# Kernel tuning notes

Measured on AMD Instinct MI355X. Metric: run time of the kernel, lower is better.

Reference implementation:

```python
import jax, jax.numpy as jnp
import numpy as np

NHEAD = 8  # from init_kwargs
EPS = 1e-5  # nn.LayerNorm default


def _ln(x, w, b):
    mu = jnp.mean(x, axis=-1, keepdims=True)
    var = jnp.mean(jnp.square(x - mu), axis=-1, keepdims=True)
    return (x - mu) * jax.lax.rsqrt(var + EPS) * w + b


def setup_inputs() -> dict:
    key = jax.random.key(0)
    L, D, FF, B, S = 4, 256, 512, 2, 4096
    ks = jax.random.split(key, 14)
    s = 0.02
    inp = {
        "seq": jax.random.normal(ks[0], (B, S, D), jnp.float32),
        "Wqkv": jax.random.normal(ks[1], (L, 3 * D, D), jnp.float32) * s,
        "bqkv": jnp.zeros((L, 3 * D), jnp.float32),
        "Wo": jax.random.normal(ks[2], (L, D, D), jnp.float32) * s,
        "bo": jnp.zeros((L, D), jnp.float32),
        "ln1_w": jnp.ones((L, D), jnp.float32),
        "ln1_b": jnp.zeros((L, D), jnp.float32),
        "ln2_w": jnp.ones((L, D), jnp.float32),
        "ln2_b": jnp.zeros((L, D), jnp.float32),
        "W1": jax.random.normal(ks[3], (L, FF, D), jnp.float32) * s,
        "b1": jnp.zeros((L, FF), jnp.float32),
        "W2": jax.random.normal(ks[4], (L, D, FF), jnp.float32) * s,
        "b2": jnp.zeros((L, D), jnp.float32),
        "n_ctx": 2048,
    }
    return inp


def _forward(seq, Wqkv, bqkv, Wo, bo, ln1_w, ln1_b, ln2_w, ln2_b, W1, b1, W2, b2, n_ctx):
    B, S, D = seq.shape
    H = NHEAD
    hd = D // H
    scale = 1.0 / np.sqrt(hd).astype(np.float32)
    x = seq
    L = Wqkv.shape[0]
    for l in range(L):
        # pre-norm self-attention block (norm_first=True)
        h = _ln(x, ln1_w[l], ln1_b[l])
        qkv = h @ Wqkv[l].T + bqkv[l]            # [B,S,3D]
        q, k, v = jnp.split(qkv, 3, axis=-1)
        q = q.reshape(B, S, H, hd)
        # Mask structure: every token (context AND query) may only attend to
        # context keys [:n_ctx] -> keys/values restricted up-front, no dense
        # [S,S] score matrix and no explicit mask needed.
        kc = k[:, :n_ctx].reshape(B, n_ctx, H, hd)
        vc = v[:, :n_ctx].reshape(B, n_ctx, H, hd)
        scores = jnp.einsum('bqhd,bkhd->bhqk', q, kc) * scale  # [B,H,S,n_ctx]
        att = jax.nn.softmax(scores, axis=-1)
        o = jnp.einsum('bhqk,bkhd->bqhd', att, vc).reshape(B, S, D)
        x = x + o @ Wo[l].T + bo[l]
        # pre-norm feed-forward block, exact (erf) GELU as in PyTorch 'gelu'
        h2 = _ln(x, ln2_w[l], ln2_b[l])
        x = x + jax.nn.gelu(h2 @ W1[l].T + b1[l], approximate=False) @ W2[l].T + b2[l]
    return x


def reference(seq, Wqkv, bqkv, Wo, bo, ln1_w, ln1_b, ln2_w, ln2_b, W1, b1, W2, b2, n_ctx):
    return _forward(seq, Wqkv, bqkv, Wo, bo, ln1_w, ln1_b, ln2_w, ln2_b, W1, b1, W2, b2, n_ctx)
```

## Files before the change

kernel.cpp:

```cpp
#include <hip/hip_runtime.h>
#include <hip/hip_bf16.h>

#define BB 2
#define SS 4096
#define DD 256
#define FFD 512
#define NLAYER 4
#define NHEAD 8
#define HD 32
#define QKVD 768
#define NROWS 8192
#define NCTX 2048

typedef unsigned short u16;
typedef unsigned int   u32;
typedef __attribute__((ext_vector_type(8))) short short8;
typedef __attribute__((ext_vector_type(4))) float f32x4;

#if __has_builtin(__builtin_amdgcn_exp2f)
#define EXP2(x) __builtin_amdgcn_exp2f(x)
#else
#define EXP2(x) exp2f(x)
#endif

__device__ __forceinline__ float bf2f(u32 u) { return __uint_as_float(u << 16); }
__device__ __forceinline__ u16 f2bu(float f) {
    union { __hip_bfloat16 h; u16 u; } cv; cv.h = __float2bfloat16(f); return cv.u;
}
__device__ __forceinline__ float gelu_f(float v) {
    return 0.5f * v * (1.0f + erff(v * 0.70710678118654752f));
}

__global__ __launch_bounds__(256) void init_kernel(
        const float* __restrict__ s0, const float* __restrict__ s1,
        const float* __restrict__ s2, const float* __restrict__ s3,
        u16* __restrict__ d0, u16* __restrict__ d1,
        u16* __restrict__ d2, u16* __restrict__ d3,
        const float* __restrict__ seq, float* __restrict__ x,
        const float* __restrict__ lw, const float* __restrict__ lb,
        u16* __restrict__ hln) {
    int blk = blockIdx.x;
    if (blk < 2048) {
        const float* s; u16* d; int base;
        if (blk < 768)       { s = s0; d = d0; base = blk; }
        else if (blk < 1024) { s = s1; d = d1; base = blk - 768; }
        else if (blk < 1536) { s = s2; d = d2; base = blk - 1024; }
        else                 { s = s3; d = d3; base = blk - 1536; }
        int i = (base * 256 + threadIdx.x) * 4;
        float4 v = *reinterpret_cast<const float4*>(s + i);
        uint2 o;
        o.x = (u32)f2bu(v.x) | ((u32)f2bu(v.y) << 16);
        o.y = (u32)f2bu(v.z) | ((u32)f2bu(v.w) << 16);
        *reinterpret_cast<uint2*>(d + i) = o;
    } else {
        int row = (blk - 2048) * 4 + (threadIdx.x >> 6);
        int lane = threadIdx.x & 63;
        int c = lane * 4;
        float4 v = *reinterpret_cast<const float4*>(seq + (size_t)row * DD + c);
        *reinterpret_cast<float4*>(x + (size_t)row * DD + c) = v;
        float s  = v.x + v.y + v.z + v.w;
        float sq = v.x*v.x + v.y*v.y + v.z*v.z + v.w*v.w;
        #pragma unroll
        for (int off = 32; off >= 1; off >>= 1) {
            s  += __shfl_xor(s, off);
            sq += __shfl_xor(sq, off);
        }
        float mu   = s * (1.0f / DD);
        float var  = sq * (1.0f / DD) - mu * mu;
        float rstd = rsqrtf(var + 1e-5f);
        float4 wv = *reinterpret_cast<const float4*>(lw + c);
        float4 bv = *reinterpret_cast<const float4*>(lb + c);
        float o0 = (v.x - mu) * rstd * wv.x + bv.x;
        float o1 = (v.y - mu) * rstd * wv.y + bv.y;
        float o2 = (v.z - mu) * rstd * wv.z + bv.z;
        float o3 = (v.w - mu) * rstd * wv.w + bv.w;
        uint2 o;
        o.x = (u32)f2bu(o0) | ((u32)f2bu(o1) << 16);
        o.y = (u32)f2bu(o2) | ((u32)f2bu(o3) << 16);
        *reinterpret_cast<uint2*>(hln + (size_t)row * DD + c) = o;
    }
}

__global__ void ln_kernel(const float* __restrict__ x, const float* __restrict__ w,
                          const float* __restrict__ b, u16* __restrict__ out) {
    int row = blockIdx.x * 4 + (threadIdx.x >> 6);
    int lane = threadIdx.x & 63;
    int c = lane * 4;
    float4 v = *reinterpret_cast<const float4*>(x + (size_t)row * DD + c);
    float s  = v.x + v.y + v.z + v.w;
    float sq = v.x*v.x + v.y*v.y + v.z*v.z + v.w*v.w;
    #pragma unroll
    for (int off = 32; off >= 1; off >>= 1) {
        s  += __shfl_xor(s, off);
        sq += __shfl_xor(sq, off);
    }
    float mu   = s * (1.0f / DD);
    float var  = sq * (1.0f / DD) - mu * mu;
    float rstd = rsqrtf(var + 1e-5f);
    float4 wv = *reinterpret_cast<const float4*>(w + c);
    float4 bv = *reinterpret_cast<const float4*>(b + c);
    float o0 = (v.x - mu) * rstd * wv.x + bv.x;
    float o1 = (v.y - mu) * rstd * wv.y + bv.y;
    float o2 = (v.z - mu) * rstd * wv.z + bv.z;
    float o3 = (v.w - mu) * rstd * wv.w + bv.w;
    uint2 o;
    o.x = (u32)f2bu(o0) | ((u32)f2bu(o1) << 16);
    o.y = (u32)f2bu(o2) | ((u32)f2bu(o3) << 16);
    *reinterpret_cast<uint2*>(out + (size_t)row * DD + c) = o;
}

template<int TM, int ACT, int RES, int WV>
__global__ __launch_bounds__(256) void mfma_gemm(
        const u16* __restrict__ A, const u16* __restrict__ W, const float* __restrict__ bias,
        float* __restrict__ outf, u16* __restrict__ outb, u16* __restrict__ vtg,
        int N, int K) {
    constexpr int MI = TM / 32;
    __shared__ __align__(16) u16 As[TM][136];
    __shared__ __align__(16) u16 Ws[64][136];
    int tid = threadIdx.x;
    int wave = tid >> 6, lane = tid & 63, la = lane & 15, quad = lane >> 4;
    int wm = (wave & 1) * (TM / 2), wn = (wave >> 1) * 32;
    int m0 = blockIdx.y * TM, n0 = blockIdx.x * 64;
    f32x4 acc[MI][2];
    #pragma unroll
    for (int mi = 0; mi < MI; mi++)
        #pragma unroll
        for (int ni = 0; ni < 2; ni++)
            acc[mi][ni] = (f32x4){0.f, 0.f, 0.f, 0.f};

    int ar = tid >> 4, ac = (tid & 15) * 8;
    for (int k0 = 0; k0 < K; k0 += 128) {
        #pragma unroll
        for (int p = 0; p < TM / 16; p++)
            *reinterpret_cast<uint4*>(&As[ar + p*16][ac]) =
                *reinterpret_cast<const uint4*>(&A[(size_t)(m0 + ar + p*16) * K + k0 + ac]);
        #pragma unroll
        for (int p = 0; p < 4; p++)
            *reinterpret_cast<uint4*>(&Ws[ar + p*16][ac]) =
                *reinterpret_cast<const uint4*>(&W[(size_t)(n0 + ar + p*16) * K + k0 + ac]);
        __syncthreads();
        #pragma unroll
        for (int kh = 0; kh < 4; kh++) {
            short8 af[MI], bf[2];
            #pragma unroll
            for (int mi = 0; mi < MI; mi++)
                af[mi] = *reinterpret_cast<const short8*>(&As[wm + mi*16 + la][kh*32 + quad*8]);
            #pragma unroll
            for (int ni = 0; ni < 2; ni++)
                bf[ni] = *reinterpret_cast<const short8*>(&Ws[wn + ni*16 + la][kh*32 + quad*8]);
            #pragma unroll
            for (int mi = 0; mi < MI; mi++)
                #pragma unroll
                for (int ni = 0; ni < 2; ni++)
                    acc[mi][ni] = __builtin_amdgcn_mfma_f32_16x16x32_bf16(af[mi], bf[ni], acc[mi][ni], 0, 0, 0);
        }
        __syncthreads();
    }

    #pragma unroll
    for (int mi = 0; mi < MI; mi++) {
        #pragma unroll
        for (int ni = 0; ni < 2; ni++) {
            int n = n0 + wn + ni*16 + la;
            float bv = bias[n];
            #pragma unroll
            for (int r = 0; r < 4; r++) {
                int m = m0 + wm + mi*16 + quad*4 + r;
                float v = acc[mi][ni][r] + bv;
                if (ACT) v = gelu_f(v);
                if (RES) outf[(size_t)m * N + n] += v;
                else     outb[(size_t)m * N + n] = f2bu(v);
            }
        }
    }

    if (WV) {
        if ((n0 >= 2*DD) && ((m0 & (SS-1)) < NCTX)) {
            int b = m0 >> 12;
            int kb = ((m0 + wm) & (SS-1)) + quad*8;
            #pragma unroll
            for (int mi = 0; mi < MI; mi++) {
                int chunk = kb + (mi >> 1)*32 + (mi & 1)*4;
                #pragma unroll
                for (int ni = 0; ni < 2; ni++) {
                    int n = n0 + wn + ni*16 + la;
                    int vc = n - 2*DD;
                    float bv = bias[n];
                    u16* dst = &vtg[((size_t)((b << 3) + (vc >> 5)) * 32 + (vc & 31)) * NCTX + chunk];
                    uint2 w;
                    w.x = (u32)f2bu(acc[mi][ni][0] + bv) | ((u32)f2bu(acc[mi][ni][1] + bv) << 16);
                    w.y = (u32)f2bu(acc[mi][ni][2] + bv) | ((u32)f2bu(acc[mi][ni][3] + bv) << 16);
                    *reinterpret_cast<uint2*>(dst) = w;
                }
            }
        }
    }
}

#define SCL2 0.2550437f
#define SH2  11.5415603f
__global__ __launch_bounds__(512, 4) void mfma_attn(const u16* __restrict__ qkv,
                                                    const u16* __restrict__ vtg,
                                                    u16* __restrict__ out) {
    __shared__ __align__(16) u16 smem[18944];
    u16 (*Ks)[128][40] = reinterpret_cast<u16(*)[128][40]>(smem);
    u16 (*Vt)[32][136] = reinterpret_cast<u16(*)[32][136]>(smem + 10240);

    int tid = threadIdx.x;
    int wv = tid >> 6, lane = tid & 63, la = lane & 15, quad = lane >> 4;
    int qw = wv & 3, ksp = wv >> 2;
    int bh = blockIdx.y, qidx = blockIdx.x;
    int b = bh >> 3, hh = bh & 7;
    size_t tokbase = (size_t)b * SS;
    int qb = qidx * 128 + qw * 32;

    short8 qf[2];
    #pragma unroll
    for (int qt = 0; qt < 2; qt++) {
        uint4 u = *reinterpret_cast<const uint4*>(
            &qkv[(tokbase + qb + qt*16 + la) * QKVD + hh*32 + quad*8]);
        union { short8 v; u16 e[8]; } qa;
        u32 w[4] = {u.x, u.y, u.z, u.w};
        #pragma unroll
        for (int i = 0; i < 4; i++) {
            qa.e[2*i]   = f2bu(bf2f(w[i] & 0xffffu) * SCL2);
            qa.e[2*i+1] = f2bu(bf2f(w[i] >> 16) * SCL2);
        }
        qf[qt] = qa.v;
    }

    f32x4 o[2][2];
    #pragma unroll
    for (int i = 0; i < 2; i++)
        #pragma unroll
        for (int j = 0; j < 2; j++) o[i][j] = (f32x4){0.f, 0.f, 0.f, 0.f};
    f32x4 l_acc[2];
    l_acc[0] = (f32x4){0.f, 0.f, 0.f, 0.f};
    l_acc[1] = (f32x4){0.f, 0.f, 0.f, 0.f};
    const f32x4 cinit = (f32x4){-SH2, -SH2, -SH2, -SH2};
    short8 onesf;
    { union { short8 v; u16 e[8]; } t;
      #pragma unroll
      for (int i = 0; i < 8; i++) t.e[i] = 0x3F80;
      onesf = t.v; }

    int sr = tid >> 2, sk = (tid & 3) * 8;
    int vr = tid >> 4, vc = (tid & 15) * 8;
    const u16* kgp0 = &qkv[(tokbase + sr) * QKVD + DD + hh*32 + sk];
    const u16* kgp1 = &qkv[(tokbase + 1024 + sr) * QKVD + DD + hh*32 + sk];
    const u16* vgp  = &vtg[((size_t)bh*32 + vr) * NCTX + vc];
    uint4 kreg0 = *reinterpret_cast<const uint4*>(kgp0);
    uint4 kreg1 = *reinterpret_cast<const uint4*>(kgp1);
    uint4 vreg0 = *reinterpret_cast<const uint4*>(vgp);
    uint4 vreg1 = *reinterpret_cast<const uint4*>(vgp + 1024);

    for (int step = 0; step < 8; step++) {
        *reinterpret_cast<uint4*>(&Ks[0][sr][sk]) = kreg0;
        *reinterpret_cast<uint4*>(&Ks[1][sr][sk]) = kreg1;
        *reinterpret_cast<uint4*>(&Vt[0][vr][vc]) = vreg0;
        *reinterpret_cast<uint4*>(&Vt[1][vr][vc]) = vreg1;
        __syncthreads();
        if (step < 7) {
            kreg0 = *reinterpret_cast<const uint4*>(kgp0 + (size_t)(step+1)*128*QKVD);
            kreg1 = *reinterpret_cast<const uint4*>(kgp1 + (size_t)(step+1)*128*QKVD);
            vreg0 = *reinterpret_cast<const uint4*>(vgp + (step+1)*128);
            vreg1 = *reinterpret_cast<const uint4*>(vgp + 1024 + (step+1)*128);
        }

        __builtin_amdgcn_s_setprio(1);
        #pragma unroll
        for (int c = 0; c < 4; c++) {
            short8 kf0 = *reinterpret_cast<const short8*>(&Ks[ksp][c*32 + la][quad*8]);
            short8 kf1 = *reinterpret_cast<const short8*>(&Ks[ksp][c*32 + 16 + la][quad*8]);
            f32x4 s00 = __builtin_amdgcn_mfma_f32_16x16x32_bf16(kf0, qf[0], cinit, 0, 0, 0);
            f32x4 s10 = __builtin_amdgcn_mfma_f32_16x16x32_bf16(kf1, qf[0], cinit, 0, 0, 0);
            f32x4 s01 = __builtin_amdgcn_mfma_f32_16x16x32_bf16(kf0, qf[1], cinit, 0, 0, 0);
            f32x4 s11 = __builtin_amdgcn_mfma_f32_16x16x32_bf16(kf1, qf[1], cinit, 0, 0, 0);

            union { uint4 u; short8 v; } pf0, pf1;
            {
                u32 a0 = __float_as_uint(EXP2(s00[0])), a1 = __float_as_uint(EXP2(s00[1]));
                u32 a2 = __float_as_uint(EXP2(s00[2])), a3 = __float_as_uint(EXP2(s00[3]));
                u32 b0 = __float_as_uint(EXP2(s10[0])), b1 = __float_as_uint(EXP2(s10[1]));
                u32 b2 = __float_as_uint(EXP2(s10[2])), b3 = __float_as_uint(EXP2(s10[3]));
                pf0.u.x = __builtin_amdgcn_perm(a1, a0, 0x07060302u);
                pf0.u.y = __builtin_amdgcn_perm(a3, a2, 0x07060302u);
                pf0.u.z = __builtin_amdgcn_perm(b1, b0, 0x07060302u);
                pf0.u.w = __builtin_amdgcn_perm(b3, b2, 0x07060302u);
            }
            {
                u32 a0 = __float_as_uint(EXP2(s01[0])), a1 = __float_as_uint(EXP2(s01[1]));
                u32 a2 = __float_as_uint(EXP2(s01[2])), a3 = __float_as_uint(EXP2(s01[3]));
                u32 b0 = __float_as_uint(EXP2(s11[0])), b1 = __float_as_uint(EXP2(s11[1]));
                u32 b2 = __float_as_uint(EXP2(s11[2])), b3 = __float_as_uint(EXP2(s11[3]));
                pf1.u.x = __builtin_amdgcn_perm(a1, a0, 0x07060302u);
                pf1.u.y = __builtin_amdgcn_perm(a3, a2, 0x07060302u);
                pf1.u.z = __builtin_amdgcn_perm(b1, b0, 0x07060302u);
                pf1.u.w = __builtin_amdgcn_perm(b3, b2, 0x07060302u);
            }

            l_acc[0] = __builtin_amdgcn_mfma_f32_16x16x32_bf16(onesf, pf0.v, l_acc[0], 0, 0, 0);
            l_acc[1] = __builtin_amdgcn_mfma_f32_16x16x32_bf16(onesf, pf1.v, l_acc[1], 0, 0, 0);

            short8 vf0 = *reinterpret_cast<const short8*>(&Vt[ksp][la][c*32 + quad*8]);
            short8 vf1 = *reinterpret_cast<const short8*>(&Vt[ksp][16 + la][c*32 + quad*8]);
            o[0][0] = __builtin_amdgcn_mfma_f32_16x16x32_bf16(vf0, pf0.v, o[0][0], 0, 0, 0);
            o[0][1] = __builtin_amdgcn_mfma_f32_16x16x32_bf16(vf0, pf1.v, o[0][1], 0, 0, 0);
            o[1][0] = __builtin_amdgcn_mfma_f32_16x16x32_bf16(vf1, pf0.v, o[1][0], 0, 0, 0);
            o[1][1] = __builtin_amdgcn_mfma_f32_16x16x32_bf16(vf1, pf1.v, o[1][1], 0, 0, 0);
        }
        __builtin_amdgcn_s_setprio(0);
        __syncthreads();
    }

    float* obuf = reinterpret_cast<float*>(smem);
    if (wv >= 4) {
        int idx = (qw * 64 + lane) * 18;
        #pragma unroll
        for (int mio = 0; mio < 2; mio++)
            #pragma unroll
            for (int qt = 0; qt < 2; qt++)
                #pragma unroll
                for (int r = 0; r < 4; r++)
                    obuf[idx + mio*8 + qt*4 + r] = o[mio][qt][r];
        obuf[idx + 16] = l_acc[0][0];
        obuf[idx + 17] = l_acc[1][0];
    }
    __syncthreads();
    if (wv < 4) {
        int idx = (qw * 64 + lane) * 18;
        #pragma unroll
        for (int mio = 0; mio < 2; mio++)
            #pragma unroll
            for (int qt = 0; qt < 2; qt++)
                #pragma unroll
                for (int r = 0; r < 4; r++)
                    o[mio][qt][r] += obuf[idx + mio*8 + qt*4 + r];
        float liq[2];
        liq[0] = 1.0f / (l_acc[0][0] + obuf[idx + 16]);
        liq[1] = 1.0f / (l_acc[1][0] + obuf[idx + 17]);
        #pragma unroll
        for (int qt = 0; qt < 2; qt++) {
            float li = liq[qt];
            size_t token = tokbase + qb + qt*16 + la;
            #pragma unroll
            for (int mio = 0; mio < 2; mio++) {
                uint2 w;
                w.x = (u32)f2bu(o[mio][qt][0] * li) | ((u32)f2bu(o[mio][qt][1] * li) << 16);
                w.y = (u32)f2bu(o[mio][qt][2] * li) | ((u32)f2bu(o[mio][qt][3] * li) << 16);
                *reinterpret_cast<uint2*>(&out[token * DD + hh*32 + mio*16 + quad*4]) = w;
            }
        }
    }
}

extern "C" void kernel_launch(void* const* d_in, const int* in_sizes, int n_in,
                              void* d_out, int out_size, void* d_ws, size_t ws_size,
                              hipStream_t stream) {
    const float* seq   = (const float*)d_in[0];
    const float* Wqkv  = (const float*)d_in[1];
    const float* bqkv  = (const float*)d_in[2];
    const float* Wo    = (const float*)d_in[3];
    const float* bo    = (const float*)d_in[4];
    const float* ln1w  = (const float*)d_in[5];
    const float* ln1b  = (const float*)d_in[6];
    const float* ln2w  = (const float*)d_in[7];
    const float* ln2b  = (const float*)d_in[8];
    const float* W1    = (const float*)d_in[9];
    const float* b1    = (const float*)d_in[10];
    const float* W2    = (const float*)d_in[11];
    const float* b2    = (const float*)d_in[12];

    float* x    = (float*)d_out;
    char* wsb   = (char*)d_ws;
    u16*  qkv   = (u16*)wsb;
    u16*  ff    = qkv;
    u16*  h     = (u16*)(wsb + 12582912);
    u16*  hln   = (u16*)(wsb + 16777216);
    u16*  wbf   = (u16*)(wsb + 20971520);
    u16*  vtg   = (u16*)(wsb + 25165824);
    u16* wqkv_b = wbf;
    u16* wo_b   = wbf + 786432;
    u16* w1_b   = wbf + 1048576;
    u16* w2_b   = wbf + 1572864;

    init_kernel<<<4096, 256, 0, stream>>>(Wqkv, Wo, W1, W2, wqkv_b, wo_b, w1_b, w2_b,
                                          seq, x, ln1w, ln1b, hln);

    for (int l = 0; l < NLAYER; l++) {
        mfma_gemm<128,0,0,1><<<dim3(QKVD/64, NROWS/128), 256, 0, stream>>>(
            hln, wqkv_b + (size_t)l*QKVD*DD, bqkv + l*QKVD, nullptr, qkv, vtg, QKVD, DD);
        mfma_attn<<<dim3(SS/128, BB*NHEAD), 512, 0, stream>>>(qkv, vtg, h);
        mfma_gemm<64,0,1,0><<<dim3(DD/64, NROWS/64), 256, 0, stream>>>(
            h, wo_b + (size_t)l*DD*DD, bo + l*DD, x, nullptr, nullptr, DD, DD);
        ln_kernel<<<NROWS/4, 256, 0, stream>>>(x, ln2w + l*DD, ln2b + l*DD, hln);
        mfma_gemm<128,1,0,0><<<dim3(FFD/64, NROWS/128), 256, 0, stream>>>(
            hln, w1_b + (size_t)l*FFD*DD, b1 + l*FFD, nullptr, ff, nullptr, FFD, DD);
        mfma_gemm<64,0,1,0><<<dim3(DD/64, NROWS/64), 256, 0, stream>>>(
            ff, w2_b + (size_t)l*DD*FFD, b2 + l*DD, x, nullptr, nullptr, DD, FFD);
        if (l < NLAYER - 1)
            ln_kernel<<<NROWS/4, 256, 0, stream>>>(x, ln1w + (l+1)*DD, ln1b + (l+1)*DD, hln);
    }
}
```

Measured before the change: 383.3 us.

## Double-buffer K/V shared tiles in attention and swizzle block-to-head mapping

The attention kernel now holds two LDS buffers for K and V tiles. The next tile is written into the other buffer while the current one is consumed, and register prefetch runs two steps ahead, which removes one barrier per iteration. Block indices are also remapped so that consecutive blocks are spread across heads, presumably for better L2 or XCD locality. LDS use doubles to about 74 KB per block, which may cut the number of resident blocks per CU.

```diff
diff --git a/kernel.cpp b/kernel.cpp
--- a/kernel.cpp
+++ b/kernel.cpp
@@ -202,14 +202,16 @@
 __global__ __launch_bounds__(512, 4) void mfma_attn(const u16* __restrict__ qkv,
                                                     const u16* __restrict__ vtg,
                                                     u16* __restrict__ out) {
-    __shared__ __align__(16) u16 smem[18944];
-    u16 (*Ks)[128][40] = reinterpret_cast<u16(*)[128][40]>(smem);
-    u16 (*Vt)[32][136] = reinterpret_cast<u16(*)[32][136]>(smem + 10240);
+    __shared__ __align__(16) u16 smem[37888];
+    u16 (*Ks)[2][128][40] = reinterpret_cast<u16(*)[2][128][40]>(smem);
+    u16 (*Vt)[2][32][136] = reinterpret_cast<u16(*)[2][32][136]>(smem + 20480);
 
     int tid = threadIdx.x;
     int wv = tid >> 6, lane = tid & 63, la = lane & 15, quad = lane >> 4;
     int qw = wv & 3, ksp = wv >> 2;
-    int bh = blockIdx.y, qidx = blockIdx.x;
+    int flat = blockIdx.y * gridDim.x + blockIdx.x;
+    int g = (flat & 7) * 64 + (flat >> 3);
+    int qidx = g & 31, bh = g >> 5;
     int b = bh >> 3, hh = bh & 7;
     size_t tokbase = (size_t)b * SS;
     int qb = qidx * 128 + qw * 32;
@@ -249,29 +251,41 @@
     const u16* kgp0 = &qkv[(tokbase + sr) * QKVD + DD + hh*32 + sk];
     const u16* kgp1 = &qkv[(tokbase + 1024 + sr) * QKVD + DD + hh*32 + sk];
     const u16* vgp  = &vtg[((size_t)bh*32 + vr) * NCTX + vc];
+
     uint4 kreg0 = *reinterpret_cast<const uint4*>(kgp0);
     uint4 kreg1 = *reinterpret_cast<const uint4*>(kgp1);
     uint4 vreg0 = *reinterpret_cast<const uint4*>(vgp);
     uint4 vreg1 = *reinterpret_cast<const uint4*>(vgp + 1024);
+    *reinterpret_cast<uint4*>(&Ks[0][0][sr][sk]) = kreg0;
+    *reinterpret_cast<uint4*>(&Ks[0][1][sr][sk]) = kreg1;
+    *reinterpret_cast<uint4*>(&Vt[0][0][vr][vc]) = vreg0;
+    *reinterpret_cast<uint4*>(&Vt[0][1][vr][vc]) = vreg1;
+    kreg0 = *reinterpret_cast<const uint4*>(kgp0 + (size_t)128*QKVD);
+    kreg1 = *reinterpret_cast<const uint4*>(kgp1 + (size_t)128*QKVD);
+    vreg0 = *reinterpret_cast<const uint4*>(vgp + 128);
+    vreg1 = *reinterpret_cast<const uint4*>(vgp + 1024 + 128);
+    __syncthreads();
 
     for (int step = 0; step < 8; step++) {
-        *reinterpret_cast<uint4*>(&Ks[0][sr][sk]) = kreg0;
-        *reinterpret_cast<uint4*>(&Ks[1][sr][sk]) = kreg1;
-        *reinterpret_cast<uint4*>(&Vt[0][vr][vc]) = vreg0;
-        *reinterpret_cast<uint4*>(&Vt[1][vr][vc]) = vreg1;
-        __syncthreads();
+        int cur = step & 1;
         if (step < 7) {
-            kreg0 = *reinterpret_cast<const uint4*>(kgp0 + (size_t)(step+1)*128*QKVD);
-            kreg1 = *reinterpret_cast<const uint4*>(kgp1 + (size_t)(step+1)*128*QKVD);
-            vreg0 = *reinterpret_cast<const uint4*>(vgp + (step+1)*128);
-            vreg1 = *reinterpret_cast<const uint4*>(vgp + 1024 + (step+1)*128);
+            *reinterpret_cast<uint4*>(&Ks[cur^1][0][sr][sk]) = kreg0;
+            *reinterpret_cast<uint4*>(&Ks[cur^1][1][sr][sk]) = kreg1;
+            *reinterpret_cast<uint4*>(&Vt[cur^1][0][vr][vc]) = vreg0;
+            *reinterpret_cast<uint4*>(&Vt[cur^1][1][vr][vc]) = vreg1;
+            if (step < 6) {
+                kreg0 = *reinterpret_cast<const uint4*>(kgp0 + (size_t)(step+2)*128*QKVD);
+                kreg1 = *reinterpret_cast<const uint4*>(kgp1 + (size_t)(step+2)*128*QKVD);
+                vreg0 = *reinterpret_cast<const uint4*>(vgp + (step+2)*128);
+                vreg1 = *reinterpret_cast<const uint4*>(vgp + 1024 + (step+2)*128);
+            }
         }
 
         __builtin_amdgcn_s_setprio(1);
         #pragma unroll
         for (int c = 0; c < 4; c++) {
-            short8 kf0 = *reinterpret_cast<const short8*>(&Ks[ksp][c*32 + la][quad*8]);
-            short8 kf1 = *reinterpret_cast<const short8*>(&Ks[ksp][c*32 + 16 + la][quad*8]);
+            short8 kf0 = *reinterpret_cast<const short8*>(&Ks[cur][ksp][c*32 + la][quad*8]);
+            short8 kf1 = *reinterpret_cast<const short8*>(&Ks[cur][ksp][c*32 + 16 + la][quad*8]);
             f32x4 s00 = __builtin_amdgcn_mfma_f32_16x16x32_bf16(kf0, qf[0], cinit, 0, 0, 0);
             f32x4 s10 = __builtin_amdgcn_mfma_f32_16x16x32_bf16(kf1, qf[0], cinit, 0, 0, 0);
             f32x4 s01 = __builtin_amdgcn_mfma_f32_16x16x32_bf16(kf0, qf[1], cinit, 0, 0, 0);
@@ -302,8 +316,8 @@
             l_acc[0] = __builtin_amdgcn_mfma_f32_16x16x32_bf16(onesf, pf0.v, l_acc[0], 0, 0, 0);
             l_acc[1] = __builtin_amdgcn_mfma_f32_16x16x32_bf16(onesf, pf1.v, l_acc[1], 0, 0, 0);
 
-            short8 vf0 = *reinterpret_cast<const short8*>(&Vt[ksp][la][c*32 + quad*8]);
-            short8 vf1 = *reinterpret_cast<const short8*>(&Vt[ksp][16 + la][c*32 + quad*8]);
+            short8 vf0 = *reinterpret_cast<const short8*>(&Vt[cur][ksp][la][c*32 + quad*8]);
+            short8 vf1 = *reinterpret_cast<const short8*>(&Vt[cur][ksp][16 + la][c*32 + quad*8]);
             o[0][0] = __builtin_amdgcn_mfma_f32_16x16x32_bf16(vf0, pf0.v, o[0][0], 0, 0, 0);
             o[0][1] = __builtin_amdgcn_mfma_f32_16x16x32_bf16(vf0, pf1.v, o[0][1], 0, 0, 0);
             o[1][0] = __builtin_amdgcn_mfma_f32_16x16x32_bf16(vf1, pf0.v, o[1][0], 0, 0, 0);
```

After: 385.1 us. About the same (+0.5%).
